# Kernel optimization log

Hardware: AMD Instinct MI355X
Metric: run time of the kernel (lower is better)

Reference implementation:

```python
import jax, jax.numpy as jnp
import numpy as np

B, N, E, C = 1, 100000, 1600000, 128


def setup_inputs() -> dict:
    key = jax.random.key(0)
    k1, k2, k3, k4 = jax.random.split(key, 4)
    x = jax.random.normal(k1, (B, N, C), dtype=jnp.float32)
    edge_index = jax.random.randint(k2, (2, E), 0, N, dtype=jnp.int32)
    W_2 = jax.random.normal(k3, (C,), dtype=jnp.float32)
    W_3 = jax.random.normal(k4, (C,), dtype=jnp.float32)
    return {"x": x, "edge_index": edge_index, "W_2": W_2, "W_3": W_3}


def reference(x, edge_index, W_2, W_3):
    # x: [B, N, C]; edge_index: [2, E] (src, dst)
    src, dst = edge_index[0], edge_index[1]
    num_nodes = x.shape[1]
    # per-edge attention weight: w[b,e] = <(x*W_3)[b,src_e], x[b,dst_e]>
    x3 = (x * W_3)[:, src, :]          # [B, E, C] gather
    x4 = x[:, dst, :]                  # [B, E, C] gather
    w = jnp.einsum('bec,bec->be', x3, x4)  # [B, E]
    # value messages with diagonal W_2 scaling, scattered to destination nodes.
    # Equivalent to out = einsum('bij,bih->bjh', dense_adj(w), x*W_2),
    # where dense_adj[src,dst] = w (to_dense_adj sums duplicate edges; so does segment_sum).
    x2 = x * W_2                       # [B, N, C]
    msg = w[..., None] * x2[:, src, :]  # [B, E, C]
    out = jax.vmap(lambda m: jax.ops.segment_sum(m, dst, num_segments=num_nodes))(msg)
    return out  # [B, N, C]
```

## Files before the change

kernel.cpp:

```cpp
#include <hip/hip_runtime.h>
#include <hip/hip_fp16.h>


#define CCH 128
#define BSHIFT 5
#define BWIDTH 32
#define MAXBIN 4096
#define CH 8192
#define LDSCAP 1280
#define SCAN_BLOCK 256
#define SCAN_ITEMS 4
#define SCAN_TILE (SCAN_BLOCK * SCAN_ITEMS)


__global__ __launch_bounds__(256) void k_pack_hist(
    const float* __restrict__ x, __half* __restrict__ xh, int n4, int nPack,
    const int* __restrict__ dst, int E, int NBIN, int* __restrict__ hist_bm)
{
    __shared__ int cnt[MAXBIN];
    const int tid = threadIdx.x;

    if (blockIdx.x < nPack) {
        const int i = blockIdx.x * 256 + tid;
        if (i < n4) {
            float4 v = reinterpret_cast<const float4*>(x)[i];
            __half2* o = reinterpret_cast<__half2*>(xh) + (size_t)i * 2;
            o[0] = __floats2half2_rn(v.x, v.y);
            o[1] = __floats2half2_rn(v.z, v.w);
        }
        return;
    }

    const int blk = blockIdx.x - nPack;
    for (int b = tid; b < NBIN; b += 256) cnt[b] = 0;
    __syncthreads();

    const int e0 = blk * CH;
    #pragma unroll
    for (int k = 0; k < CH / 1024; ++k) {
        const int g = (e0 >> 2) + k * 256 + tid;
        const int e = g << 2;
        if (e >= E) continue;
        if (e + 4 <= E) {
            const int4 d4 = reinterpret_cast<const int4*>(dst)[g];
            atomicAdd(&cnt[d4.x >> BSHIFT], 1);
            atomicAdd(&cnt[d4.y >> BSHIFT], 1);
            atomicAdd(&cnt[d4.z >> BSHIFT], 1);
            atomicAdd(&cnt[d4.w >> BSHIFT], 1);
        } else {
            for (int ee = e; ee < E; ++ee) atomicAdd(&cnt[dst[ee] >> BSHIFT], 1);
        }
    }
    __syncthreads();
    int* hb = hist_bm + (size_t)blk * NBIN;
    for (int b = tid; b < NBIN; b += 256) hb[b] = cnt[b];
}


__global__ void k_pscan1(const int* __restrict__ hist_bm, int M, int NBIN, int NBLK,
                         int* __restrict__ partial, int* __restrict__ blocksum) {
    __shared__ int sdata[SCAN_BLOCK];
    const int base = blockIdx.x * SCAN_TILE;
    const int t = threadIdx.x;
    int v[SCAN_ITEMS];
    int local = 0;
    #pragma unroll
    for (int k = 0; k < SCAN_ITEMS; ++k) {
        int idx = base + t * SCAN_ITEMS + k;
        int val = 0;
        if (idx < M) {
            int bin = idx / NBLK, blk = idx % NBLK;
            val = hist_bm[(size_t)blk * NBIN + bin];
        }
        v[k] = val;
        local += val;
    }
    sdata[t] = local;
    __syncthreads();
    #pragma unroll
    for (int off = 1; off < SCAN_BLOCK; off <<= 1) {
        int val = (t >= off) ? sdata[t - off] : 0;
        __syncthreads();
        sdata[t] += val;
        __syncthreads();
    }
    const int incl = sdata[t];
    int run = incl - local;
    if (t == SCAN_BLOCK - 1) blocksum[blockIdx.x] = incl;
    #pragma unroll
    for (int k = 0; k < SCAN_ITEMS; ++k) {
        int idx = base + t * SCAN_ITEMS + k;
        if (idx < M) partial[idx] = run;
        run += v[k];
    }
}

__global__ void k_scan2(int* __restrict__ blocksum, int nb) {
    __shared__ int sdata[1024];
    const int t = threadIdx.x;
    const int v = (t < nb) ? blocksum[t] : 0;
    sdata[t] = v;
    __syncthreads();
    for (int off = 1; off < 1024; off <<= 1) {
        int val = (t >= off) ? sdata[t - off] : 0;
        __syncthreads();
        sdata[t] += val;
        __syncthreads();
    }
    if (t < nb) blocksum[t] = sdata[t] - v;
}


__global__ __launch_bounds__(256) void k_place(
    const int* __restrict__ src, const int* __restrict__ dst, int E, int NBIN, int NBLK,
    const int* __restrict__ partial, const int* __restrict__ blocksum,
    unsigned int* __restrict__ coarse)
{
    __shared__ int lcur[MAXBIN];
    const int blk = blockIdx.x;
    const int tid = threadIdx.x;
    for (int b = tid; b < NBIN; b += 256) {
        const size_t idx = (size_t)b * NBLK + blk;
        lcur[b] = partial[idx] + blocksum[idx / SCAN_TILE];
    }
    __syncthreads();

    const int e0 = blk * CH;
    #pragma unroll
    for (int k = 0; k < CH / 1024; ++k) {
        const int g = (e0 >> 2) + k * 256 + tid;
        const int e = g << 2;
        if (e >= E) continue;
        if (e + 4 <= E) {
            const int4 d4 = reinterpret_cast<const int4*>(dst)[g];
            const int4 s4 = reinterpret_cast<const int4*>(src)[g];
            int p;
            p = atomicAdd(&lcur[d4.x >> BSHIFT], 1);
            coarse[p] = (unsigned)s4.x | ((unsigned)(d4.x & (BWIDTH - 1)) << 17);
            p = atomicAdd(&lcur[d4.y >> BSHIFT], 1);
            coarse[p] = (unsigned)s4.y | ((unsigned)(d4.y & (BWIDTH - 1)) << 17);
            p = atomicAdd(&lcur[d4.z >> BSHIFT], 1);
            coarse[p] = (unsigned)s4.z | ((unsigned)(d4.z & (BWIDTH - 1)) << 17);
            p = atomicAdd(&lcur[d4.w >> BSHIFT], 1);
            coarse[p] = (unsigned)s4.w | ((unsigned)(d4.w & (BWIDTH - 1)) << 17);
        } else {
            for (int ee = e; ee < E; ++ee) {
                const int d = dst[ee], s = src[ee];
                int p = atomicAdd(&lcur[d >> BSHIFT], 1);
                coarse[p] = (unsigned)s | ((unsigned)(d & (BWIDTH - 1)) << 17);
            }
        }
    }
}


__global__ __launch_bounds__(256) void k_sort_accum(
    const __half* __restrict__ xh,
    const float* __restrict__ W2,
    const float* __restrict__ W3,
    const unsigned int* __restrict__ coarse,
    const int* __restrict__ partial, const int* __restrict__ blocksum,
    int NBIN, int NBLK, int E, int N,
    float* __restrict__ out)
{
    __shared__ unsigned int raw[LDSCAP];
    __shared__ int srcl[LDSCAP];
    __shared__ int cnt[BWIDTH], offs[BWIDTH], cur[BWIDTH];

    const int bin = blockIdx.x;
    const int tid = threadIdx.x;
    const size_t i0 = (size_t)bin * NBLK;
    const int beg = partial[i0] + blocksum[i0 / SCAN_TILE];
    const int end = (bin + 1 < NBIN)
        ? partial[i0 + NBLK] + blocksum[(i0 + NBLK) / SCAN_TILE] : E;
    const int mtot = end - beg;
    const int m = (mtot < LDSCAP) ? mtot : LDSCAP;

    if (tid < BWIDTH) cnt[tid] = 0;
    __syncthreads();

    for (int i = tid; i < m; i += 256) {
        unsigned u = coarse[beg + i];
        raw[i] = u;
        atomicAdd(&cnt[u >> 17], 1);
    }
    __syncthreads();

    if (tid < BWIDTH) {
        int c = cnt[tid];
        int v = c;
        #pragma unroll
        for (int d2 = 1; d2 < BWIDTH; d2 <<= 1) {
            int t2 = __shfl_up(v, d2, 64);
            if (tid >= d2) v += t2;
        }
        offs[tid] = v - c;
        cur[tid]  = v - c;
    }
    __syncthreads();

    for (int i = tid; i < m; i += 256) {
        unsigned u = raw[i];
        int p = atomicAdd(&cur[u >> 17], 1);
        srcl[p] = (int)(u & 0x1FFFFu);
    }
    __syncthreads();

    const int lane = tid & 63;
    const int grp  = lane >> 4;
    const int sl   = lane & 15;
    const int gid  = (tid >> 6) * 4 + grp;

    const float4 w3a = *reinterpret_cast<const float4*>(W3 + sl * 8);
    const float4 w3b = *reinterpret_cast<const float4*>(W3 + sl * 8 + 4);
    const float4 w2a = *reinterpret_cast<const float4*>(W2 + sl * 8);
    const float4 w2b = *reinterpret_cast<const float4*>(W2 + sl * 8 + 4);

    const char* xb = (const char*)xh;
    const int choff = sl << 4;

    #pragma unroll
    for (int i = 0; i < BWIDTH / 16; ++i) {
        const int dl = gid * (BWIDTH / 16) + i;
        const int node = (bin << BSHIFT) + dl;
        if (node < N) {
            union { int4 i4; __half2 h[4]; } uD;
            uD.i4 = *reinterpret_cast<const int4*>(xb + (((size_t)node) << 8) + choff);
            const float2 e0 = __half22float2(uD.h[0]);
            const float2 e1 = __half22float2(uD.h[1]);
            const float2 e2 = __half22float2(uD.h[2]);
            const float2 e3 = __half22float2(uD.h[3]);
            const float4 va = make_float4(w3a.x * e0.x, w3a.y * e0.y,
                                          w3a.z * e1.x, w3a.w * e1.y);
            const float4 vb = make_float4(w3b.x * e2.x, w3b.y * e2.y,
                                          w3b.z * e3.x, w3b.w * e3.y);

            float4 accA = make_float4(0.f, 0.f, 0.f, 0.f);
            float4 accB = make_float4(0.f, 0.f, 0.f, 0.f);

            const int b0 = offs[dl];
            const int c  = cnt[dl];

            int j = 0;
            for (; j + 4 <= c; j += 4) {
                const int s0 = srcl[b0 + j];
                const int s1 = srcl[b0 + j + 1];
                const int s2 = srcl[b0 + j + 2];
                const int s3 = srcl[b0 + j + 3];
                union { int4 i4; __half2 h[4]; } u0, u1, u2, u3;
                u0.i4 = *reinterpret_cast<const int4*>(xb + (((size_t)s0) << 8) + choff);
                u1.i4 = *reinterpret_cast<const int4*>(xb + (((size_t)s1) << 8) + choff);
                u2.i4 = *reinterpret_cast<const int4*>(xb + (((size_t)s2) << 8) + choff);
                u3.i4 = *reinterpret_cast<const int4*>(xb + (((size_t)s3) << 8) + choff);
                const float2 f00 = __half22float2(u0.h[0]);
                const float2 f01 = __half22float2(u0.h[1]);
                const float2 f02 = __half22float2(u0.h[2]);
                const float2 f03 = __half22float2(u0.h[3]);
                const float2 f10 = __half22float2(u1.h[0]);
                const float2 f11 = __half22float2(u1.h[1]);
                const float2 f12 = __half22float2(u1.h[2]);
                const float2 f13 = __half22float2(u1.h[3]);
                const float2 f20 = __half22float2(u2.h[0]);
                const float2 f21 = __half22float2(u2.h[1]);
                const float2 f22 = __half22float2(u2.h[2]);
                const float2 f23 = __half22float2(u2.h[3]);
                const float2 f30 = __half22float2(u3.h[0]);
                const float2 f31 = __half22float2(u3.h[1]);
                const float2 f32 = __half22float2(u3.h[2]);
                const float2 f33 = __half22float2(u3.h[3]);
                float p0 = f00.x * va.x + f00.y * va.y + f01.x * va.z + f01.y * va.w
                         + f02.x * vb.x + f02.y * vb.y + f03.x * vb.z + f03.y * vb.w;
                float p1 = f10.x * va.x + f10.y * va.y + f11.x * va.z + f11.y * va.w
                         + f12.x * vb.x + f12.y * vb.y + f13.x * vb.z + f13.y * vb.w;
                float p2 = f20.x * va.x + f20.y * va.y + f21.x * va.z + f21.y * va.w
                         + f22.x * vb.x + f22.y * vb.y + f23.x * vb.z + f23.y * vb.w;
                float p3 = f30.x * va.x + f30.y * va.y + f31.x * va.z + f31.y * va.w
                         + f32.x * vb.x + f32.y * vb.y + f33.x * vb.z + f33.y * vb.w;
                #pragma unroll
                for (int off = 1; off < 16; off <<= 1) {
                    p0 += __shfl_xor(p0, off, 64);
                    p1 += __shfl_xor(p1, off, 64);
                    p2 += __shfl_xor(p2, off, 64);
                    p3 += __shfl_xor(p3, off, 64);
                }
                accA.x += p0 * f00.x + p1 * f10.x + p2 * f20.x + p3 * f30.x;
                accA.y += p0 * f00.y + p1 * f10.y + p2 * f20.y + p3 * f30.y;
                accA.z += p0 * f01.x + p1 * f11.x + p2 * f21.x + p3 * f31.x;
                accA.w += p0 * f01.y + p1 * f11.y + p2 * f21.y + p3 * f31.y;
                accB.x += p0 * f02.x + p1 * f12.x + p2 * f22.x + p3 * f32.x;
                accB.y += p0 * f02.y + p1 * f12.y + p2 * f22.y + p3 * f32.y;
                accB.z += p0 * f03.x + p1 * f13.x + p2 * f23.x + p3 * f33.x;
                accB.w += p0 * f03.y + p1 * f13.y + p2 * f23.y + p3 * f33.y;
            }
            for (; j < c; ++j) {
                const int s0 = srcl[b0 + j];
                union { int4 i4; __half2 h[4]; } u0;
                u0.i4 = *reinterpret_cast<const int4*>(xb + (((size_t)s0) << 8) + choff);
                const float2 f0 = __half22float2(u0.h[0]);
                const float2 f1 = __half22float2(u0.h[1]);
                const float2 f2 = __half22float2(u0.h[2]);
                const float2 f3 = __half22float2(u0.h[3]);
                float p = f0.x * va.x + f0.y * va.y + f1.x * va.z + f1.y * va.w
                        + f2.x * vb.x + f2.y * vb.y + f3.x * vb.z + f3.y * vb.w;
                #pragma unroll
                for (int off = 1; off < 16; off <<= 1) p += __shfl_xor(p, off, 64);
                accA.x += p * f0.x;
                accA.y += p * f0.y;
                accA.z += p * f1.x;
                accA.w += p * f1.y;
                accB.x += p * f2.x;
                accB.y += p * f2.y;
                accB.z += p * f3.x;
                accB.w += p * f3.y;
            }
            for (int i2 = LDSCAP; i2 < mtot; ++i2) {
                const unsigned u = coarse[beg + i2];
                if ((int)(u >> 17) != dl) continue;
                const int s0 = (int)(u & 0x1FFFFu);
                union { int4 i4; __half2 h[4]; } u0;
                u0.i4 = *reinterpret_cast<const int4*>(xb + (((size_t)s0) << 8) + choff);
                const float2 f0 = __half22float2(u0.h[0]);
                const float2 f1 = __half22float2(u0.h[1]);
                const float2 f2 = __half22float2(u0.h[2]);
                const float2 f3 = __half22float2(u0.h[3]);
                float p = f0.x * va.x + f0.y * va.y + f1.x * va.z + f1.y * va.w
                        + f2.x * vb.x + f2.y * vb.y + f3.x * vb.z + f3.y * vb.w;
                #pragma unroll
                for (int off = 1; off < 16; off <<= 1) p += __shfl_xor(p, off, 64);
                accA.x += p * f0.x;
                accA.y += p * f0.y;
                accA.z += p * f1.x;
                accA.w += p * f1.y;
                accB.x += p * f2.x;
                accB.y += p * f2.y;
                accB.z += p * f3.x;
                accB.w += p * f3.y;
            }

            accA.x *= w2a.x; accA.y *= w2a.y; accA.z *= w2a.z; accA.w *= w2a.w;
            accB.x *= w2b.x; accB.y *= w2b.y; accB.z *= w2b.z; accB.w *= w2b.w;
            float* orow = out + (size_t)node * CCH + sl * 8;
            *reinterpret_cast<float4*>(orow)     = accA;
            *reinterpret_cast<float4*>(orow + 4) = accB;
        }
    }
}


__global__ __launch_bounds__(256) void edge_gather_scatter(
    const float* __restrict__ x, const int* __restrict__ edge_index,
    const float* __restrict__ W2, const float* __restrict__ W3,
    float* __restrict__ out, int E)
{
    const int e    = (blockIdx.x * blockDim.x + threadIdx.x) >> 6;
    const int lane = threadIdx.x & 63;
    if (e >= E) return;
    const int s = edge_index[e];
    const int d = edge_index[E + e];
    const float2 xs = *reinterpret_cast<const float2*>(x + (size_t)s * CCH + lane * 2);
    const float2 xd = *reinterpret_cast<const float2*>(x + (size_t)d * CCH + lane * 2);
    const float2 w3 = *reinterpret_cast<const float2*>(W3 + lane * 2);
    const float2 w2 = *reinterpret_cast<const float2*>(W2 + lane * 2);
    float p = xs.x * w3.x * xd.x + xs.y * w3.y * xd.y;
    #pragma unroll
    for (int off = 32; off > 0; off >>= 1) p += __shfl_xor(p, off, 64);
    float* o = out + (size_t)d * CCH + lane * 2;
    atomicAdd(o,     p * xs.x * w2.x);
    atomicAdd(o + 1, p * xs.y * w2.y);
}


extern "C" void kernel_launch(void* const* d_in, const int* in_sizes, int n_in,
                              void* d_out, int out_size, void* d_ws, size_t ws_size,
                              hipStream_t stream) {
    const float* x          = (const float*)d_in[0];
    const int*   edge_index = (const int*)  d_in[1];
    const float* W2         = (const float*)d_in[2];
    const float* W3         = (const float*)d_in[3];
    float*       out        = (float*)d_out;

    const int E = in_sizes[1] / 2;
    const int N = out_size / CCH;
    const int* src = edge_index;
    const int* dst = edge_index + E;

    const int NBIN = (N + BWIDTH - 1) >> BSHIFT;
    const int NBLK = (E + CH - 1) / CH;
    const long long Mll = (long long)NBIN * NBLK;
    const int M = (int)Mll;
    const int nb1 = (M + SCAN_TILE - 1) / SCAN_TILE;

    const size_t xh_bytes = (size_t)N * CCH * 2;
    const size_t need = xh_bytes + (size_t)E * 4 + 2 * (size_t)M * 4 + 1024 * 4;

    const bool aligned16 = (((uintptr_t)src & 15) == 0) && (((uintptr_t)dst & 15) == 0);

    if (N <= (1 << 17) && NBIN <= MAXBIN && Mll <= (1LL << 20) && nb1 <= 1024 &&
        aligned16 && ws_size >= need) {
        char* base = (char*)d_ws;
        __half* xh       = (__half*)base;        base += xh_bytes;
        unsigned* coarse = (unsigned*)base;      base += (size_t)E * 4;
        int* hist_bm     = (int*)base;           base += (size_t)M * 4;
        int* partial     = (int*)base;           base += (size_t)M * 4;
        int* blocksum    = (int*)base;

        const int n4 = N * CCH / 4;
        const int nPack = (n4 + 255) / 256;

        k_pack_hist<<<nPack + NBLK, 256, 0, stream>>>(x, xh, n4, nPack,
                                                      dst, E, NBIN, hist_bm);
        k_pscan1<<<nb1, SCAN_BLOCK, 0, stream>>>(hist_bm, M, NBIN, NBLK, partial, blocksum);
        k_scan2<<<1, 1024, 0, stream>>>(blocksum, nb1);
        k_place<<<NBLK, 256, 0, stream>>>(src, dst, E, NBIN, NBLK,
                                          partial, blocksum, coarse);
        k_sort_accum<<<NBIN, 256, 0, stream>>>(xh, W2, W3, coarse,
                                               partial, blocksum,
                                               NBIN, NBLK, E, N, out);
        return;
    }

    hipMemsetAsync(d_out, 0, (size_t)out_size * sizeof(float), stream);
    const int grid = (E * 64 + 255) / 256;
    edge_gather_scatter<<<grid, 256, 0, stream>>>(x, edge_index, W2, W3, out, E);
}
```

Measured before the change: 125.5 us.

## Tile bin-major histogram scan through LDS and deepen gather batching in accumulate

The first-level scan now loads a 16-bin by NBLK tile of the block-major histogram into shared memory, so global reads stay coalesced and each block's offsets match whole bins, replacing the strided index/divide access. The sort-accumulate kernel uses per-wave counters for its LDS counting sort to cut atomic contention. It also prefetches the destination rows before the sort phase and batches eight source-row gathers per iteration for more memory parallelism, with a two-blocks-per-CU launch bound. A new NBLK cap adds a guard on the fast path, and the wider batch raises register pressure.

```diff
diff --git a/kernel.cpp b/kernel.cpp
--- a/kernel.cpp
+++ b/kernel.cpp
@@ -8,9 +8,8 @@
 #define MAXBIN 4096
 #define CH 8192
 #define LDSCAP 1280
-#define SCAN_BLOCK 256
-#define SCAN_ITEMS 4
-#define SCAN_TILE (SCAN_BLOCK * SCAN_ITEMS)
+#define TBINS 16
+#define NBLKCAP 256
 
 
 __global__ __launch_bounds__(256) void k_pack_hist(
@@ -57,28 +56,38 @@
 }
 
 
-__global__ void k_pscan1(const int* __restrict__ hist_bm, int M, int NBIN, int NBLK,
-                         int* __restrict__ partial, int* __restrict__ blocksum) {
-    __shared__ int sdata[SCAN_BLOCK];
-    const int base = blockIdx.x * SCAN_TILE;
+__global__ __launch_bounds__(256) void k_pscan1(
+    const int* __restrict__ hist_bm, int NBIN, int NBLK,
+    int* __restrict__ partial, int* __restrict__ blocksum)
+{
+    __shared__ int tile[TBINS][NBLKCAP + 1];
+    __shared__ int sdata[256];
     const int t = threadIdx.x;
-    int v[SCAN_ITEMS];
+    const int B0 = blockIdx.x * TBINS;
+
+    for (int g = t; g < TBINS * (NBLKCAP + 1); g += 256)
+        (&tile[0][0])[g] = 0;
+    __syncthreads();
+
+    for (int g = t; g < NBLK * TBINS; g += 256) {
+        const int blk = g >> 4;
+        const int tb  = g & (TBINS - 1);
+        const int bin = B0 + tb;
+        if (bin < NBIN) tile[tb][blk] = hist_bm[(size_t)blk * NBIN + bin];
+    }
+    __syncthreads();
+
+    const int tb  = t >> 4;
+    const int bk0 = (t & 15) * 16;
+    int v[16];
     int local = 0;
     #pragma unroll
-    for (int k = 0; k < SCAN_ITEMS; ++k) {
-        int idx = base + t * SCAN_ITEMS + k;
-        int val = 0;
-        if (idx < M) {
-            int bin = idx / NBLK, blk = idx % NBLK;
-            val = hist_bm[(size_t)blk * NBIN + bin];
-        }
-        v[k] = val;
-        local += val;
-    }
+    for (int k = 0; k < 16; ++k) { v[k] = tile[tb][bk0 + k]; local += v[k]; }
+
     sdata[t] = local;
     __syncthreads();
     #pragma unroll
-    for (int off = 1; off < SCAN_BLOCK; off <<= 1) {
+    for (int off = 1; off < 256; off <<= 1) {
         int val = (t >= off) ? sdata[t - off] : 0;
         __syncthreads();
         sdata[t] += val;
@@ -86,12 +95,16 @@
     }
     const int incl = sdata[t];
     int run = incl - local;
-    if (t == SCAN_BLOCK - 1) blocksum[blockIdx.x] = incl;
-    #pragma unroll
-    for (int k = 0; k < SCAN_ITEMS; ++k) {
-        int idx = base + t * SCAN_ITEMS + k;
-        if (idx < M) partial[idx] = run;
-        run += v[k];
+    if (t == 255) blocksum[blockIdx.x] = incl;
+
+    const int bin = B0 + tb;
+    if (bin < NBIN) {
+        #pragma unroll
+        for (int k = 0; k < 16; ++k) {
+            const int blk = bk0 + k;
+            if (blk < NBLK) partial[(size_t)bin * NBLK + blk] = run;
+            run += v[k];
+        }
     }
 }
 
@@ -120,8 +133,7 @@
     const int blk = blockIdx.x;
     const int tid = threadIdx.x;
     for (int b = tid; b < NBIN; b += 256) {
-        const size_t idx = (size_t)b * NBLK + blk;
-        lcur[b] = partial[idx] + blocksum[idx / SCAN_TILE];
+        lcur[b] = partial[(size_t)b * NBLK + blk] + blocksum[b / TBINS];
     }
     __syncthreads();
 
@@ -154,7 +166,7 @@
 }
 
 
-__global__ __launch_bounds__(256) void k_sort_accum(
+__global__ __launch_bounds__(256, 2) void k_sort_accum(
     const __half* __restrict__ xh,
     const float* __restrict__ W2,
     const float* __restrict__ W3,
@@ -165,184 +177,204 @@
 {
     __shared__ unsigned int raw[LDSCAP];
     __shared__ int srcl[LDSCAP];
-    __shared__ int cnt[BWIDTH], offs[BWIDTH], cur[BWIDTH];
-
-    const int bin = blockIdx.x;
-    const int tid = threadIdx.x;
+    __shared__ int cnt4[4][BWIDTH];
+    __shared__ int cur4[4][BWIDTH];
+    __shared__ int offs[BWIDTH], cnt[BWIDTH];
+
+    const int bin  = blockIdx.x;
+    const int tid  = threadIdx.x;
+    const int wv   = tid >> 6;
+    const int lane = tid & 63;
+    const int grp  = lane >> 4;
+    const int sl   = lane & 15;
+    const int gid  = wv * 4 + grp;
+    const int choff = sl << 4;
+    const char* xb = (const char*)xh;
+
+    union H { int4 i4; __half2 h[4]; };
+
+    const int node0 = (bin << BSHIFT) + gid * 2;
+    const int node1 = node0 + 1;
+    H uD0, uD1;
+    uD0.i4 = make_int4(0, 0, 0, 0);
+    uD1.i4 = make_int4(0, 0, 0, 0);
+    if (node0 < N) uD0.i4 = *reinterpret_cast<const int4*>(xb + (((size_t)node0) << 8) + choff);
+    if (node1 < N) uD1.i4 = *reinterpret_cast<const int4*>(xb + (((size_t)node1) << 8) + choff);
+
     const size_t i0 = (size_t)bin * NBLK;
-    const int beg = partial[i0] + blocksum[i0 / SCAN_TILE];
+    const int beg = partial[i0] + blocksum[bin / TBINS];
     const int end = (bin + 1 < NBIN)
-        ? partial[i0 + NBLK] + blocksum[(i0 + NBLK) / SCAN_TILE] : E;
+        ? partial[i0 + NBLK] + blocksum[(bin + 1) / TBINS] : E;
     const int mtot = end - beg;
     const int m = (mtot < LDSCAP) ? mtot : LDSCAP;
 
-    if (tid < BWIDTH) cnt[tid] = 0;
+    if (tid < 4 * BWIDTH) (&cnt4[0][0])[tid] = 0;
     __syncthreads();
 
     for (int i = tid; i < m; i += 256) {
         unsigned u = coarse[beg + i];
         raw[i] = u;
-        atomicAdd(&cnt[u >> 17], 1);
+        atomicAdd(&cnt4[wv][u >> 17], 1);
     }
     __syncthreads();
 
     if (tid < BWIDTH) {
-        int c = cnt[tid];
-        int v = c;
+        const int c0 = cnt4[0][tid], c1 = cnt4[1][tid];
+        const int c2 = cnt4[2][tid], c3 = cnt4[3][tid];
+        const int tot = c0 + c1 + c2 + c3;
+        int v = tot;
         #pragma unroll
         for (int d2 = 1; d2 < BWIDTH; d2 <<= 1) {
             int t2 = __shfl_up(v, d2, 64);
             if (tid >= d2) v += t2;
         }
-        offs[tid] = v - c;
-        cur[tid]  = v - c;
+        const int ex = v - tot;
+        offs[tid] = ex;
+        cnt[tid]  = tot;
+        cur4[0][tid] = ex;
+        cur4[1][tid] = ex + c0;
+        cur4[2][tid] = ex + c0 + c1;
+        cur4[3][tid] = ex + c0 + c1 + c2;
     }
     __syncthreads();
 
     for (int i = tid; i < m; i += 256) {
-        unsigned u = raw[i];
-        int p = atomicAdd(&cur[u >> 17], 1);
+        const unsigned u = raw[i];
+        const int p = atomicAdd(&cur4[wv][u >> 17], 1);
         srcl[p] = (int)(u & 0x1FFFFu);
     }
     __syncthreads();
-
-    const int lane = tid & 63;
-    const int grp  = lane >> 4;
-    const int sl   = lane & 15;
-    const int gid  = (tid >> 6) * 4 + grp;
 
     const float4 w3a = *reinterpret_cast<const float4*>(W3 + sl * 8);
     const float4 w3b = *reinterpret_cast<const float4*>(W3 + sl * 8 + 4);
     const float4 w2a = *reinterpret_cast<const float4*>(W2 + sl * 8);
     const float4 w2b = *reinterpret_cast<const float4*>(W2 + sl * 8 + 4);
 
-    const char* xb = (const char*)xh;
-    const int choff = sl << 4;
-
-    #pragma unroll
-    for (int i = 0; i < BWIDTH / 16; ++i) {
-        const int dl = gid * (BWIDTH / 16) + i;
-        const int node = (bin << BSHIFT) + dl;
-        if (node < N) {
-            union { int4 i4; __half2 h[4]; } uD;
-            uD.i4 = *reinterpret_cast<const int4*>(xb + (((size_t)node) << 8) + choff);
-            const float2 e0 = __half22float2(uD.h[0]);
-            const float2 e1 = __half22float2(uD.h[1]);
-            const float2 e2 = __half22float2(uD.h[2]);
-            const float2 e3 = __half22float2(uD.h[3]);
-            const float4 va = make_float4(w3a.x * e0.x, w3a.y * e0.y,
-                                          w3a.z * e1.x, w3a.w * e1.y);
-            const float4 vb = make_float4(w3b.x * e2.x, w3b.y * e2.y,
-                                          w3b.z * e3.x, w3b.w * e3.y);
-
-            float4 accA = make_float4(0.f, 0.f, 0.f, 0.f);
-            float4 accB = make_float4(0.f, 0.f, 0.f, 0.f);
-
-            const int b0 = offs[dl];
-            const int c  = cnt[dl];
-
-            int j = 0;
-            for (; j + 4 <= c; j += 4) {
-                const int s0 = srcl[b0 + j];
-                const int s1 = srcl[b0 + j + 1];
-                const int s2 = srcl[b0 + j + 2];
-                const int s3 = srcl[b0 + j + 3];
-                union { int4 i4; __half2 h[4]; } u0, u1, u2, u3;
-                u0.i4 = *reinterpret_cast<const int4*>(xb + (((size_t)s0) << 8) + choff);
-                u1.i4 = *reinterpret_cast<const int4*>(xb + (((size_t)s1) << 8) + choff);
-                u2.i4 = *reinterpret_cast<const int4*>(xb + (((size_t)s2) << 8) + choff);
-                u3.i4 = *reinterpret_cast<const int4*>(xb + (((size_t)s3) << 8) + choff);
-                const float2 f00 = __half22float2(u0.h[0]);
-                const float2 f01 = __half22float2(u0.h[1]);
-                const float2 f02 = __half22float2(u0.h[2]);
-                const float2 f03 = __half22float2(u0.h[3]);
-                const float2 f10 = __half22float2(u1.h[0]);
-                const float2 f11 = __half22float2(u1.h[1]);
-                const float2 f12 = __half22float2(u1.h[2]);
-                const float2 f13 = __half22float2(u1.h[3]);
-                const float2 f20 = __half22float2(u2.h[0]);
-                const float2 f21 = __half22float2(u2.h[1]);
-                const float2 f22 = __half22float2(u2.h[2]);
-                const float2 f23 = __half22float2(u2.h[3]);
-                const float2 f30 = __half22float2(u3.h[0]);
-                const float2 f31 = __half22float2(u3.h[1]);
-                const float2 f32 = __half22float2(u3.h[2]);
-                const float2 f33 = __half22float2(u3.h[3]);
-                float p0 = f00.x * va.x + f00.y * va.y + f01.x * va.z + f01.y * va.w
-                         + f02.x * vb.x + f02.y * vb.y + f03.x * vb.z + f03.y * vb.w;
-                float p1 = f10.x * va.x + f10.y * va.y + f11.x * va.z + f11.y * va.w
-                         + f12.x * vb.x + f12.y * vb.y + f13.x * vb.z + f13.y * vb.w;
-                float p2 = f20.x * va.x + f20.y * va.y + f21.x * va.z + f21.y * va.w
-                         + f22.x * vb.x + f22.y * vb.y + f23.x * vb.z + f23.y * vb.w;
-                float p3 = f30.x * va.x + f30.y * va.y + f31.x * va.z + f31.y * va.w
-                         + f32.x * vb.x + f32.y * vb.y + f33.x * vb.z + f33.y * vb.w;
+    #pragma unroll
+    for (int i = 0; i < 2; ++i) {
+        const int node = (i == 0) ? node0 : node1;
+        if (node >= N) continue;
+        const int dl = gid * 2 + i;
+        const H uD = (i == 0) ? uD0 : uD1;
+
+        const float2 e0 = __half22float2(uD.h[0]);
+        const float2 e1 = __half22float2(uD.h[1]);
+        const float2 e2 = __half22float2(uD.h[2]);
+        const float2 e3 = __half22float2(uD.h[3]);
+        const float4 va = make_float4(w3a.x * e0.x, w3a.y * e0.y,
+                                      w3a.z * e1.x, w3a.w * e1.y);
+        const float4 vb = make_float4(w3b.x * e2.x, w3b.y * e2.y,
+                                      w3b.z * e3.x, w3b.w * e3.y);
+
+        float4 accA = make_float4(0.f, 0.f, 0.f, 0.f);
+        float4 accB = make_float4(0.f, 0.f, 0.f, 0.f);
+
+        const int b0 = offs[dl];
+        const int c  = cnt[dl];
+
+        int j = 0;
+        for (; j + 8 <= c; j += 8) {
+            H q[8];
+            #pragma unroll
+            for (int k = 0; k < 8; ++k)
+                q[k].i4 = *reinterpret_cast<const int4*>(
+                    xb + (((size_t)srcl[b0 + j + k]) << 8) + choff);
+            float2 f0[8], f1[8], f2[8], f3[8];
+            float p[8];
+            #pragma unroll
+            for (int k = 0; k < 8; ++k) {
+                f0[k] = __half22float2(q[k].h[0]);
+                f1[k] = __half22float2(q[k].h[1]);
+                f2[k] = __half22float2(q[k].h[2]);
+                f3[k] = __half22float2(q[k].h[3]);
+                p[k] = f0[k].x * va.x + f0[k].y * va.y + f1[k].x * va.z + f1[k].y * va.w
+                     + f2[k].x * vb.x + f2[k].y * vb.y + f3[k].x * vb.z + f3[k].y * vb.w;
+            }
+            #pragma unroll
+            for (int off = 1; off < 16; off <<= 1) {
                 #pragma unroll
-                for (int off = 1; off < 16; off <<= 1) {
-                    p0 += __shfl_xor(p0, off, 64);
-                    p1 += __shfl_xor(p1, off, 64);
-                    p2 += __shfl_xor(p2, off, 64);
-                    p3 += __shfl_xor(p3, off, 64);
-                }
-                accA.x += p0 * f00.x + p1 * f10.x + p2 * f20.x + p3 * f30.x;
-                accA.y += p0 * f00.y + p1 * f10.y + p2 * f20.y + p3 * f30.y;
-                accA.z += p0 * f01.x + p1 * f11.x + p2 * f21.x + p3 * f31.x;
-                accA.w += p0 * f01.y + p1 * f11.y + p2 * f21.y + p3 * f31.y;
-                accB.x += p0 * f02.x + p1 * f12.x + p2 * f22.x + p3 * f32.x;
-                accB.y += p0 * f02.y + p1 * f12.y + p2 * f22.y + p3 * f32.y;
-                accB.z += p0 * f03.x + p1 * f13.x + p2 * f23.x + p3 * f33.x;
-                accB.w += p0 * f03.y + p1 * f13.y + p2 * f23.y + p3 * f33.y;
-            }
-            for (; j < c; ++j) {
-                const int s0 = srcl[b0 + j];
-                union { int4 i4; __half2 h[4]; } u0;
-                u0.i4 = *reinterpret_cast<const int4*>(xb + (((size_t)s0) << 8) + choff);
-                const float2 f0 = __half22float2(u0.h[0]);
-                const float2 f1 = __half22float2(u0.h[1]);
-                const float2 f2 = __half22float2(u0.h[2]);
-                const float2 f3 = __half22float2(u0.h[3]);
-                float p = f0.x * va.x + f0.y * va.y + f1.x * va.z + f1.y * va.w
-                        + f2.x * vb.x + f2.y * vb.y + f3.x * vb.z + f3.y * vb.w;
+                for (int k = 0; k < 8; ++k) p[k] += __shfl_xor(p[k], off, 64);
+            }
+            #pragma unroll
+            for (int k = 0; k < 8; ++k) {
+                accA.x += p[k] * f0[k].x; accA.y += p[k] * f0[k].y;
+                accA.z += p[k] * f1[k].x; accA.w += p[k] * f1[k].y;
+                accB.x += p[k] * f2[k].x; accB.y += p[k] * f2[k].y;
+                accB.z += p[k] * f3[k].x; accB.w += p[k] * f3[k].y;
+            }
+        }
+        for (; j + 4 <= c; j += 4) {
+            H q[4];
+            #pragma unroll
+            for (int k = 0; k < 4; ++k)
+                q[k].i4 = *reinterpret_cast<const int4*>(
+                    xb + (((size_t)srcl[b0 + j + k]) << 8) + choff);
+            float2 f0[4], f1[4], f2[4], f3[4];
+            float p[4];
+            #pragma unroll
+            for (int k = 0; k < 4; ++k) {
+                f0[k] = __half22float2(q[k].h[0]);
+                f1[k] = __half22float2(q[k].h[1]);
+                f2[k] = __half22float2(q[k].h[2]);
+                f3[k] = __half22float2(q[k].h[3]);
+                p[k] = f0[k].x * va.x + f0[k].y * va.y + f1[k].x * va.z + f1[k].y * va.w
+                     + f2[k].x * vb.x + f2[k].y * vb.y + f3[k].x * vb.z + f3[k].y * vb.w;
+            }
+            #pragma unroll
+            for (int off = 1; off < 16; off <<= 1) {
                 #pragma unroll
-                for (int off = 1; off < 16; off <<= 1) p += __shfl_xor(p, off, 64);
-                accA.x += p * f0.x;
-                accA.y += p * f0.y;
-                accA.z += p * f1.x;
-                accA.w += p * f1.y;
-                accB.x += p * f2.x;
-                accB.y += p * f2.y;
-                accB.z += p * f3.x;
-                accB.w += p * f3.y;
-            }
-            for (int i2 = LDSCAP; i2 < mtot; ++i2) {
-                const unsigned u = coarse[beg + i2];
-                if ((int)(u >> 17) != dl) continue;
-                const int s0 = (int)(u & 0x1FFFFu);
-                union { int4 i4; __half2 h[4]; } u0;
-                u0.i4 = *reinterpret_cast<const int4*>(xb + (((size_t)s0) << 8) + choff);
-                const float2 f0 = __half22float2(u0.h[0]);
-                const float2 f1 = __half22float2(u0.h[1]);
-                const float2 f2 = __half22float2(u0.h[2]);
-                const float2 f3 = __half22float2(u0.h[3]);
-                float p = f0.x * va.x + f0.y * va.y + f1.x * va.z + f1.y * va.w
-                        + f2.x * vb.x + f2.y * vb.y + f3.x * vb.z + f3.y * vb.w;
-                #pragma unroll
-                for (int off = 1; off < 16; off <<= 1) p += __shfl_xor(p, off, 64);
-                accA.x += p * f0.x;
-                accA.y += p * f0.y;
-                accA.z += p * f1.x;
-                accA.w += p * f1.y;
-                accB.x += p * f2.x;
-                accB.y += p * f2.y;
-                accB.z += p * f3.x;
-                accB.w += p * f3.y;
-            }
-
-            accA.x *= w2a.x; accA.y *= w2a.y; accA.z *= w2a.z; accA.w *= w2a.w;
-            accB.x *= w2b.x; accB.y *= w2b.y; accB.z *= w2b.z; accB.w *= w2b.w;
-            float* orow = out + (size_t)node * CCH + sl * 8;
-            *reinterpret_cast<float4*>(orow)     = accA;
-            *reinterpret_cast<float4*>(orow + 4) = accB;
-        }
+                for (int k = 0; k < 4; ++k) p[k] += __shfl_xor(p[k], off, 64);
+            }
+            #pragma unroll
+            for (int k = 0; k < 4; ++k) {
+                accA.x += p[k] * f0[k].x; accA.y += p[k] * f0[k].y;
+                accA.z += p[k] * f1[k].x; accA.w += p[k] * f1[k].y;
+                accB.x += p[k] * f2[k].x; accB.y += p[k] * f2[k].y;
+                accB.z += p[k] * f3[k].x; accB.w += p[k] * f3[k].y;
+            }
+        }
+        for (; j < c; ++j) {
+            H u0;
+            u0.i4 = *reinterpret_cast<const int4*>(
+                xb + (((size_t)srcl[b0 + j]) << 8) + choff);
+            const float2 f0 = __half22float2(u0.h[0]);
+            const float2 f1 = __half22float2(u0.h[1]);
+            const float2 f2 = __half22float2(u0.h[2]);
+            const float2 f3 = __half22float2(u0.h[3]);
+            float p = f0.x * va.x + f0.y * va.y + f1.x * va.z + f1.y * va.w
+                    + f2.x * vb.x + f2.y * vb.y + f3.x * vb.z + f3.y * vb.w;
+            #pragma unroll
+            for (int off = 1; off < 16; off <<= 1) p += __shfl_xor(p, off, 64);
+            accA.x += p * f0.x; accA.y += p * f0.y;
+            accA.z += p * f1.x; accA.w += p * f1.y;
+            accB.x += p * f2.x; accB.y += p * f2.y;
+            accB.z += p * f3.x; accB.w += p * f3.y;
+        }
+        for (int i2 = LDSCAP; i2 < mtot; ++i2) {
+            const unsigned u = coarse[beg + i2];
+            if ((int)(u >> 17) != dl) continue;
+            H u0;
+            u0.i4 = *reinterpret_cast<const int4*>(
+                xb + (((size_t)(u & 0x1FFFFu)) << 8) + choff);
+            const float2 f0 = __half22float2(u0.h[0]);
+            const float2 f1 = __half22float2(u0.h[1]);
+            const float2 f2 = __half22float2(u0.h[2]);
+            const float2 f3 = __half22float2(u0.h[3]);
+            float p = f0.x * va.x + f0.y * va.y + f1.x * va.z + f1.y * va.w
+                    + f2.x * vb.x + f2.y * vb.y + f3.x * vb.z + f3.y * vb.w;
+            #pragma unroll
+            for (int off = 1; off < 16; off <<= 1) p += __shfl_xor(p, off, 64);
+            accA.x += p * f0.x; accA.y += p * f0.y;
+            accA.z += p * f1.x; accA.w += p * f1.y;
+            accB.x += p * f2.x; accB.y += p * f2.y;
+            accB.z += p * f3.x; accB.w += p * f3.y;
+        }
+
+        accA.x *= w2a.x; accA.y *= w2a.y; accA.z *= w2a.z; accA.w *= w2a.w;
+        accB.x *= w2b.x; accB.y *= w2b.y; accB.z *= w2b.z; accB.w *= w2b.w;
+        float* orow = out + (size_t)node * CCH + sl * 8;
+        *reinterpret_cast<float4*>(orow)     = accA;
+        *reinterpret_cast<float4*>(orow + 4) = accB;
     }
 }
 
@@ -388,15 +420,15 @@
     const int NBLK = (E + CH - 1) / CH;
     const long long Mll = (long long)NBIN * NBLK;
     const int M = (int)Mll;
-    const int nb1 = (M + SCAN_TILE - 1) / SCAN_TILE;
+    const int nb1 = (NBIN + TBINS - 1) / TBINS;
 
     const size_t xh_bytes = (size_t)N * CCH * 2;
     const size_t need = xh_bytes + (size_t)E * 4 + 2 * (size_t)M * 4 + 1024 * 4;
 
     const bool aligned16 = (((uintptr_t)src & 15) == 0) && (((uintptr_t)dst & 15) == 0);
 
-    if (N <= (1 << 17) && NBIN <= MAXBIN && Mll <= (1LL << 20) && nb1 <= 1024 &&
-        aligned16 && ws_size >= need) {
+    if (N <= (1 << 17) && NBIN <= MAXBIN && NBLK <= NBLKCAP && Mll <= (1LL << 20) &&
+        nb1 <= 1024 && aligned16 && ws_size >= need) {
         char* base = (char*)d_ws;
         __half* xh       = (__half*)base;        base += xh_bytes;
         unsigned* coarse = (unsigned*)base;      base += (size_t)E * 4;
@@ -409,7 +441,7 @@
 
         k_pack_hist<<<nPack + NBLK, 256, 0, stream>>>(x, xh, n4, nPack,
                                                       dst, E, NBIN, hist_bm);
-        k_pscan1<<<nb1, SCAN_BLOCK, 0, stream>>>(hist_bm, M, NBIN, NBLK, partial, blocksum);
+        k_pscan1<<<nb1, 256, 0, stream>>>(hist_bm, NBIN, NBLK, partial, blocksum);
         k_scan2<<<1, 1024, 0, stream>>>(blocksum, nb1);
         k_place<<<NBLK, 256, 0, stream>>>(src, dst, E, NBIN, NBLK,
                                           partial, blocksum, coarse);
```

Result: slower. 130.4 us (+3.9%).

## Replace two-pass scan with single-pass decoupled look-back scan and prefetch dst rows

Applied to the files above, without the earlier changes.

The two-kernel prefix scan (per-tile scan plus a single-block scan of block sums) becomes one kernel. It stages a 16-bin by NBLK tile of the histogram in LDS for coalesced reads and chains tiles with a decoupled look-back over a status array, which is zeroed by an added memset. Consumers now read one scanned array instead of adding partial and blocksum. The accumulate kernel issues its two destination-row loads before the LDS bucket sort so their latency overlaps it. The look-back relies on forward progress across earlier blocks, and a new NBLK cap narrows when the fast path is taken.

```diff
diff --git a/kernel.cpp b/kernel.cpp
--- a/kernel.cpp
+++ b/kernel.cpp
@@ -8,9 +8,8 @@
 #define MAXBIN 4096
 #define CH 8192
 #define LDSCAP 1280
-#define SCAN_BLOCK 256
-#define SCAN_ITEMS 4
-#define SCAN_TILE (SCAN_BLOCK * SCAN_ITEMS)
+#define TBINS 16
+#define NBLKCAP 256
 
 
 __global__ __launch_bounds__(256) void k_pack_hist(
@@ -57,72 +56,89 @@
 }
 
 
-__global__ void k_pscan1(const int* __restrict__ hist_bm, int M, int NBIN, int NBLK,
-                         int* __restrict__ partial, int* __restrict__ blocksum) {
-    __shared__ int sdata[SCAN_BLOCK];
-    const int base = blockIdx.x * SCAN_TILE;
+__global__ __launch_bounds__(256) void k_pscan(
+    const int* __restrict__ hist_bm, int NBIN, int NBLK, int E_unused,
+    int* __restrict__ scanned, unsigned int* __restrict__ status)
+{
+    __shared__ int tile[TBINS][NBLKCAP + 1];
+    __shared__ int sdata[256];
+    __shared__ int sbase;
     const int t = threadIdx.x;
-    int v[SCAN_ITEMS];
+    const int B0 = blockIdx.x * TBINS;
+
+    for (int g = t; g < TBINS * (NBLKCAP + 1); g += 256)
+        (&tile[0][0])[g] = 0;
+    __syncthreads();
+
+    for (int g = t; g < NBLK * TBINS; g += 256) {
+        const int blk = g >> 4;
+        const int tb  = g & (TBINS - 1);
+        const int bin = B0 + tb;
+        if (bin < NBIN) tile[tb][blk] = hist_bm[(size_t)blk * NBIN + bin];
+    }
+    __syncthreads();
+
+    const int tb  = t >> 4;
+    const int bk0 = (t & 15) * 16;
+    int v[16];
     int local = 0;
     #pragma unroll
-    for (int k = 0; k < SCAN_ITEMS; ++k) {
-        int idx = base + t * SCAN_ITEMS + k;
-        int val = 0;
-        if (idx < M) {
-            int bin = idx / NBLK, blk = idx % NBLK;
-            val = hist_bm[(size_t)blk * NBIN + bin];
-        }
-        v[k] = val;
-        local += val;
-    }
+    for (int k = 0; k < 16; ++k) { v[k] = tile[tb][bk0 + k]; local += v[k]; }
+
     sdata[t] = local;
     __syncthreads();
     #pragma unroll
-    for (int off = 1; off < SCAN_BLOCK; off <<= 1) {
+    for (int off = 1; off < 256; off <<= 1) {
         int val = (t >= off) ? sdata[t - off] : 0;
         __syncthreads();
         sdata[t] += val;
         __syncthreads();
     }
     const int incl = sdata[t];
-    int run = incl - local;
-    if (t == SCAN_BLOCK - 1) blocksum[blockIdx.x] = incl;
-    #pragma unroll
-    for (int k = 0; k < SCAN_ITEMS; ++k) {
-        int idx = base + t * SCAN_ITEMS + k;
-        if (idx < M) partial[idx] = run;
-        run += v[k];
-    }
-}
-
-__global__ void k_scan2(int* __restrict__ blocksum, int nb) {
-    __shared__ int sdata[1024];
-    const int t = threadIdx.x;
-    const int v = (t < nb) ? blocksum[t] : 0;
-    sdata[t] = v;
-    __syncthreads();
-    for (int off = 1; off < 1024; off <<= 1) {
-        int val = (t >= off) ? sdata[t - off] : 0;
-        __syncthreads();
-        sdata[t] += val;
-        __syncthreads();
-    }
-    if (t < nb) blocksum[t] = sdata[t] - v;
+    const int total = sdata[255];
+
+    if (t == 0) {
+        __hip_atomic_store(&status[blockIdx.x], (1u << 30) | (unsigned)total,
+                           __ATOMIC_RELAXED, __HIP_MEMORY_SCOPE_AGENT);
+        int base = 0;
+        for (int j = (int)blockIdx.x - 1; j >= 0; --j) {
+            unsigned w;
+            do {
+                w = __hip_atomic_load(&status[j], __ATOMIC_RELAXED,
+                                      __HIP_MEMORY_SCOPE_AGENT);
+            } while ((w >> 30) == 0u);
+            base += (int)(w & 0x3FFFFFFFu);
+            if ((w >> 30) == 2u) break;
+        }
+        __hip_atomic_store(&status[blockIdx.x],
+                           (2u << 30) | (unsigned)(base + total),
+                           __ATOMIC_RELAXED, __HIP_MEMORY_SCOPE_AGENT);
+        sbase = base;
+    }
+    __syncthreads();
+
+    int run = sbase + (incl - local);
+    const int bin = B0 + tb;
+    if (bin < NBIN) {
+        #pragma unroll
+        for (int k = 0; k < 16; ++k) {
+            const int blk = bk0 + k;
+            if (blk < NBLK) scanned[(size_t)bin * NBLK + blk] = run;
+            run += v[k];
+        }
+    }
 }
 
 
 __global__ __launch_bounds__(256) void k_place(
     const int* __restrict__ src, const int* __restrict__ dst, int E, int NBIN, int NBLK,
-    const int* __restrict__ partial, const int* __restrict__ blocksum,
-    unsigned int* __restrict__ coarse)
+    const int* __restrict__ scanned, unsigned int* __restrict__ coarse)
 {
     __shared__ int lcur[MAXBIN];
     const int blk = blockIdx.x;
     const int tid = threadIdx.x;
-    for (int b = tid; b < NBIN; b += 256) {
-        const size_t idx = (size_t)b * NBLK + blk;
-        lcur[b] = partial[idx] + blocksum[idx / SCAN_TILE];
-    }
+    for (int b = tid; b < NBIN; b += 256)
+        lcur[b] = scanned[(size_t)b * NBLK + blk];
     __syncthreads();
 
     const int e0 = blk * CH;
@@ -159,7 +175,7 @@
     const float* __restrict__ W2,
     const float* __restrict__ W3,
     const unsigned int* __restrict__ coarse,
-    const int* __restrict__ partial, const int* __restrict__ blocksum,
+    const int* __restrict__ scanned,
     int NBIN, int NBLK, int E, int N,
     float* __restrict__ out)
 {
@@ -167,12 +183,28 @@
     __shared__ int srcl[LDSCAP];
     __shared__ int cnt[BWIDTH], offs[BWIDTH], cur[BWIDTH];
 
-    const int bin = blockIdx.x;
-    const int tid = threadIdx.x;
+    const int bin  = blockIdx.x;
+    const int tid  = threadIdx.x;
+    const int lane = tid & 63;
+    const int grp  = lane >> 4;
+    const int sl   = lane & 15;
+    const int gid  = (tid >> 6) * 4 + grp;
+    const int choff = sl << 4;
+    const char* xb = (const char*)xh;
+
+    union H { int4 i4; __half2 h[4]; };
+
+    const int node0 = (bin << BSHIFT) + gid * 2;
+    const int node1 = node0 + 1;
+    H uD0, uD1;
+    uD0.i4 = make_int4(0, 0, 0, 0);
+    uD1.i4 = make_int4(0, 0, 0, 0);
+    if (node0 < N) uD0.i4 = *reinterpret_cast<const int4*>(xb + (((size_t)node0) << 8) + choff);
+    if (node1 < N) uD1.i4 = *reinterpret_cast<const int4*>(xb + (((size_t)node1) << 8) + choff);
+
     const size_t i0 = (size_t)bin * NBLK;
-    const int beg = partial[i0] + blocksum[i0 / SCAN_TILE];
-    const int end = (bin + 1 < NBIN)
-        ? partial[i0 + NBLK] + blocksum[(i0 + NBLK) / SCAN_TILE] : E;
+    const int beg = scanned[i0];
+    const int end = (bin + 1 < NBIN) ? scanned[i0 + NBLK] : E;
     const int mtot = end - beg;
     const int m = (mtot < LDSCAP) ? mtot : LDSCAP;
 
@@ -200,149 +232,132 @@
     __syncthreads();
 
     for (int i = tid; i < m; i += 256) {
-        unsigned u = raw[i];
-        int p = atomicAdd(&cur[u >> 17], 1);
+        const unsigned u = raw[i];
+        const int p = atomicAdd(&cur[u >> 17], 1);
         srcl[p] = (int)(u & 0x1FFFFu);
     }
     __syncthreads();
-
-    const int lane = tid & 63;
-    const int grp  = lane >> 4;
-    const int sl   = lane & 15;
-    const int gid  = (tid >> 6) * 4 + grp;
 
     const float4 w3a = *reinterpret_cast<const float4*>(W3 + sl * 8);
     const float4 w3b = *reinterpret_cast<const float4*>(W3 + sl * 8 + 4);
     const float4 w2a = *reinterpret_cast<const float4*>(W2 + sl * 8);
     const float4 w2b = *reinterpret_cast<const float4*>(W2 + sl * 8 + 4);
 
-    const char* xb = (const char*)xh;
-    const int choff = sl << 4;
-
-    #pragma unroll
-    for (int i = 0; i < BWIDTH / 16; ++i) {
-        const int dl = gid * (BWIDTH / 16) + i;
-        const int node = (bin << BSHIFT) + dl;
-        if (node < N) {
-            union { int4 i4; __half2 h[4]; } uD;
-            uD.i4 = *reinterpret_cast<const int4*>(xb + (((size_t)node) << 8) + choff);
-            const float2 e0 = __half22float2(uD.h[0]);
-            const float2 e1 = __half22float2(uD.h[1]);
-            const float2 e2 = __half22float2(uD.h[2]);
-            const float2 e3 = __half22float2(uD.h[3]);
-            const float4 va = make_float4(w3a.x * e0.x, w3a.y * e0.y,
-                                          w3a.z * e1.x, w3a.w * e1.y);
-            const float4 vb = make_float4(w3b.x * e2.x, w3b.y * e2.y,
-                                          w3b.z * e3.x, w3b.w * e3.y);
-
-            float4 accA = make_float4(0.f, 0.f, 0.f, 0.f);
-            float4 accB = make_float4(0.f, 0.f, 0.f, 0.f);
-
-            const int b0 = offs[dl];
-            const int c  = cnt[dl];
-
-            int j = 0;
-            for (; j + 4 <= c; j += 4) {
-                const int s0 = srcl[b0 + j];
-                const int s1 = srcl[b0 + j + 1];
-                const int s2 = srcl[b0 + j + 2];
-                const int s3 = srcl[b0 + j + 3];
-                union { int4 i4; __half2 h[4]; } u0, u1, u2, u3;
-                u0.i4 = *reinterpret_cast<const int4*>(xb + (((size_t)s0) << 8) + choff);
-                u1.i4 = *reinterpret_cast<const int4*>(xb + (((size_t)s1) << 8) + choff);
-                u2.i4 = *reinterpret_cast<const int4*>(xb + (((size_t)s2) << 8) + choff);
-                u3.i4 = *reinterpret_cast<const int4*>(xb + (((size_t)s3) << 8) + choff);
-                const float2 f00 = __half22float2(u0.h[0]);
-                const float2 f01 = __half22float2(u0.h[1]);
-                const float2 f02 = __half22float2(u0.h[2]);
-                const float2 f03 = __half22float2(u0.h[3]);
-                const float2 f10 = __half22float2(u1.h[0]);
-                const float2 f11 = __half22float2(u1.h[1]);
-                const float2 f12 = __half22float2(u1.h[2]);
-                const float2 f13 = __half22float2(u1.h[3]);
-                const float2 f20 = __half22float2(u2.h[0]);
-                const float2 f21 = __half22float2(u2.h[1]);
-                const float2 f22 = __half22float2(u2.h[2]);
-                const float2 f23 = __half22float2(u2.h[3]);
-                const float2 f30 = __half22float2(u3.h[0]);
-                const float2 f31 = __half22float2(u3.h[1]);
-                const float2 f32 = __half22float2(u3.h[2]);
-                const float2 f33 = __half22float2(u3.h[3]);
-                float p0 = f00.x * va.x + f00.y * va.y + f01.x * va.z + f01.y * va.w
-                         + f02.x * vb.x + f02.y * vb.y + f03.x * vb.z + f03.y * vb.w;
-                float p1 = f10.x * va.x + f10.y * va.y + f11.x * va.z + f11.y * va.w
-                         + f12.x * vb.x + f12.y * vb.y + f13.x * vb.z + f13.y * vb.w;
-                float p2 = f20.x * va.x + f20.y * va.y + f21.x * va.z + f21.y * va.w
-                         + f22.x * vb.x + f22.y * vb.y + f23.x * vb.z + f23.y * vb.w;
-                float p3 = f30.x * va.x + f30.y * va.y + f31.x * va.z + f31.y * va.w
-                         + f32.x * vb.x + f32.y * vb.y + f33.x * vb.z + f33.y * vb.w;
-                #pragma unroll
-                for (int off = 1; off < 16; off <<= 1) {
-                    p0 += __shfl_xor(p0, off, 64);
-                    p1 += __shfl_xor(p1, off, 64);
-                    p2 += __shfl_xor(p2, off, 64);
-                    p3 += __shfl_xor(p3, off, 64);
-                }
-                accA.x += p0 * f00.x + p1 * f10.x + p2 * f20.x + p3 * f30.x;
-                accA.y += p0 * f00.y + p1 * f10.y + p2 * f20.y + p3 * f30.y;
-                accA.z += p0 * f01.x + p1 * f11.x + p2 * f21.x + p3 * f31.x;
-                accA.w += p0 * f01.y + p1 * f11.y + p2 * f21.y + p3 * f31.y;
-                accB.x += p0 * f02.x + p1 * f12.x + p2 * f22.x + p3 * f32.x;
-                accB.y += p0 * f02.y + p1 * f12.y + p2 * f22.y + p3 * f32.y;
-                accB.z += p0 * f03.x + p1 * f13.x + p2 * f23.x + p3 * f33.x;
-                accB.w += p0 * f03.y + p1 * f13.y + p2 * f23.y + p3 * f33.y;
+    #pragma unroll
+    for (int i = 0; i < 2; ++i) {
+        const int node = (i == 0) ? node0 : node1;
+        if (node >= N) continue;
+        const int dl = gid * 2 + i;
+        const H uD = (i == 0) ? uD0 : uD1;
+
+        const float2 e0 = __half22float2(uD.h[0]);
+        const float2 e1 = __half22float2(uD.h[1]);
+        const float2 e2 = __half22float2(uD.h[2]);
+        const float2 e3 = __half22float2(uD.h[3]);
+        const float4 va = make_float4(w3a.x * e0.x, w3a.y * e0.y,
+                                      w3a.z * e1.x, w3a.w * e1.y);
+        const float4 vb = make_float4(w3b.x * e2.x, w3b.y * e2.y,
+                                      w3b.z * e3.x, w3b.w * e3.y);
+
+        float4 accA = make_float4(0.f, 0.f, 0.f, 0.f);
+        float4 accB = make_float4(0.f, 0.f, 0.f, 0.f);
+
+        const int b0 = offs[dl];
+        const int c  = cnt[dl];
+
+        int j = 0;
+        for (; j + 4 <= c; j += 4) {
+            const int s0 = srcl[b0 + j];
+            const int s1 = srcl[b0 + j + 1];
+            const int s2 = srcl[b0 + j + 2];
+            const int s3 = srcl[b0 + j + 3];
+            H u0, u1, u2, u3;
+            u0.i4 = *reinterpret_cast<const int4*>(xb + (((size_t)s0) << 8) + choff);
+            u1.i4 = *reinterpret_cast<const int4*>(xb + (((size_t)s1) << 8) + choff);
+            u2.i4 = *reinterpret_cast<const int4*>(xb + (((size_t)s2) << 8) + choff);
+            u3.i4 = *reinterpret_cast<const int4*>(xb + (((size_t)s3) << 8) + choff);
+            const float2 f00 = __half22float2(u0.h[0]);
+            const float2 f01 = __half22float2(u0.h[1]);
+            const float2 f02 = __half22float2(u0.h[2]);
+            const float2 f03 = __half22float2(u0.h[3]);
+            const float2 f10 = __half22float2(u1.h[0]);
+            const float2 f11 = __half22float2(u1.h[1]);
+            const float2 f12 = __half22float2(u1.h[2]);
+            const float2 f13 = __half22float2(u1.h[3]);
+            const float2 f20 = __half22float2(u2.h[0]);
+            const float2 f21 = __half22float2(u2.h[1]);
+            const float2 f22 = __half22float2(u2.h[2]);
+            const float2 f23 = __half22float2(u2.h[3]);
+            const float2 f30 = __half22float2(u3.h[0]);
+            const float2 f31 = __half22float2(u3.h[1]);
+            const float2 f32 = __half22float2(u3.h[2]);
+            const float2 f33 = __half22float2(u3.h[3]);
+            float p0 = f00.x * va.x + f00.y * va.y + f01.x * va.z + f01.y * va.w
+                     + f02.x * vb.x + f02.y * vb.y + f03.x * vb.z + f03.y * vb.w;
+            float p1 = f10.x * va.x + f10.y * va.y + f11.x * va.z + f11.y * va.w
+                     + f12.x * vb.x + f12.y * vb.y + f13.x * vb.z + f13.y * vb.w;
+            float p2 = f20.x * va.x + f20.y * va.y + f21.x * va.z + f21.y * va.w
+                     + f22.x * vb.x + f22.y * vb.y + f23.x * vb.z + f23.y * vb.w;
+            float p3 = f30.x * va.x + f30.y * va.y + f31.x * va.z + f31.y * va.w
+                     + f32.x * vb.x + f32.y * vb.y + f33.x * vb.z + f33.y * vb.w;
+            #pragma unroll
+            for (int off = 1; off < 16; off <<= 1) {
+                p0 += __shfl_xor(p0, off, 64);
+                p1 += __shfl_xor(p1, off, 64);
+                p2 += __shfl_xor(p2, off, 64);
+                p3 += __shfl_xor(p3, off, 64);
             }
-            for (; j < c; ++j) {
-                const int s0 = srcl[b0 + j];
-                union { int4 i4; __half2 h[4]; } u0;
-                u0.i4 = *reinterpret_cast<const int4*>(xb + (((size_t)s0) << 8) + choff);
-                const float2 f0 = __half22float2(u0.h[0]);
-                const float2 f1 = __half22float2(u0.h[1]);
-                const float2 f2 = __half22float2(u0.h[2]);
-                const float2 f3 = __half22float2(u0.h[3]);
-                float p = f0.x * va.x + f0.y * va.y + f1.x * va.z + f1.y * va.w
-                        + f2.x * vb.x + f2.y * vb.y + f3.x * vb.z + f3.y * vb.w;
-                #pragma unroll
-                for (int off = 1; off < 16; off <<= 1) p += __shfl_xor(p, off, 64);
-                accA.x += p * f0.x;
-                accA.y += p * f0.y;
-                accA.z += p * f1.x;
-                accA.w += p * f1.y;
-                accB.x += p * f2.x;
-                accB.y += p * f2.y;
-                accB.z += p * f3.x;
-                accB.w += p * f3.y;
-            }
-            for (int i2 = LDSCAP; i2 < mtot; ++i2) {
-                const unsigned u = coarse[beg + i2];
-                if ((int)(u >> 17) != dl) continue;
-                const int s0 = (int)(u & 0x1FFFFu);
-                union { int4 i4; __half2 h[4]; } u0;
-                u0.i4 = *reinterpret_cast<const int4*>(xb + (((size_t)s0) << 8) + choff);
-                const float2 f0 = __half22float2(u0.h[0]);
-                const float2 f1 = __half22float2(u0.h[1]);
-                const float2 f2 = __half22float2(u0.h[2]);
-                const float2 f3 = __half22float2(u0.h[3]);
-                float p = f0.x * va.x + f0.y * va.y + f1.x * va.z + f1.y * va.w
-                        + f2.x * vb.x + f2.y * vb.y + f3.x * vb.z + f3.y * vb.w;
-                #pragma unroll
-                for (int off = 1; off < 16; off <<= 1) p += __shfl_xor(p, off, 64);
-                accA.x += p * f0.x;
-                accA.y += p * f0.y;
-                accA.z += p * f1.x;
-                accA.w += p * f1.y;
-                accB.x += p * f2.x;
-                accB.y += p * f2.y;
-                accB.z += p * f3.x;
-                accB.w += p * f3.y;
-            }
-
-            accA.x *= w2a.x; accA.y *= w2a.y; accA.z *= w2a.z; accA.w *= w2a.w;
-            accB.x *= w2b.x; accB.y *= w2b.y; accB.z *= w2b.z; accB.w *= w2b.w;
-            float* orow = out + (size_t)node * CCH + sl * 8;
-            *reinterpret_cast<float4*>(orow)     = accA;
-            *reinterpret_cast<float4*>(orow + 4) = accB;
-        }
+            accA.x += p0 * f00.x + p1 * f10.x + p2 * f20.x + p3 * f30.x;
+            accA.y += p0 * f00.y + p1 * f10.y + p2 * f20.y + p3 * f30.y;
+            accA.z += p0 * f01.x + p1 * f11.x + p2 * f21.x + p3 * f31.x;
+            accA.w += p0 * f01.y + p1 * f11.y + p2 * f21.y + p3 * f31.y;
+            accB.x += p0 * f02.x + p1 * f12.x + p2 * f22.x + p3 * f32.x;
+            accB.y += p0 * f02.y + p1 * f12.y + p2 * f22.y + p3 * f32.y;
+            accB.z += p0 * f03.x + p1 * f13.x + p2 * f23.x + p3 * f33.x;
+            accB.w += p0 * f03.y + p1 * f13.y + p2 * f23.y + p3 * f33.y;
+        }
+        for (; j < c; ++j) {
+            H u0;
+            u0.i4 = *reinterpret_cast<const int4*>(
+                xb + (((size_t)srcl[b0 + j]) << 8) + choff);
+            const float2 f0 = __half22float2(u0.h[0]);
+            const float2 f1 = __half22float2(u0.h[1]);
+            const float2 f2 = __half22float2(u0.h[2]);
+            const float2 f3 = __half22float2(u0.h[3]);
+            float p = f0.x * va.x + f0.y * va.y + f1.x * va.z + f1.y * va.w
+                    + f2.x * vb.x + f2.y * vb.y + f3.x * vb.z + f3.y * vb.w;
+            #pragma unroll
+            for (int off = 1; off < 16; off <<= 1) p += __shfl_xor(p, off, 64);
+            accA.x += p * f0.x; accA.y += p * f0.y;
+            accA.z += p * f1.x; accA.w += p * f1.y;
+            accB.x += p * f2.x; accB.y += p * f2.y;
+            accB.z += p * f3.x; accB.w += p * f3.y;
+        }
+        for (int i2 = LDSCAP; i2 < mtot; ++i2) {
+            const unsigned u = coarse[beg + i2];
+            if ((int)(u >> 17) != dl) continue;
+            H u0;
+            u0.i4 = *reinterpret_cast<const int4*>(
+                xb + (((size_t)(u & 0x1FFFFu)) << 8) + choff);
+            const float2 f0 = __half22float2(u0.h[0]);
+            const float2 f1 = __half22float2(u0.h[1]);
+            const float2 f2 = __half22float2(u0.h[2]);
+            const float2 f3 = __half22float2(u0.h[3]);
+            float p = f0.x * va.x + f0.y * va.y + f1.x * va.z + f1.y * va.w
+                    + f2.x * vb.x + f2.y * vb.y + f3.x * vb.z + f3.y * vb.w;
+            #pragma unroll
+            for (int off = 1; off < 16; off <<= 1) p += __shfl_xor(p, off, 64);
+            accA.x += p * f0.x; accA.y += p * f0.y;
+            accA.z += p * f1.x; accA.w += p * f1.y;
+            accB.x += p * f2.x; accB.y += p * f2.y;
+            accB.z += p * f3.x; accB.w += p * f3.y;
+        }
+
+        accA.x *= w2a.x; accA.y *= w2a.y; accA.z *= w2a.z; accA.w *= w2a.w;
+        accB.x *= w2b.x; accB.y *= w2b.y; accB.z *= w2b.z; accB.w *= w2b.w;
+        float* orow = out + (size_t)node * CCH + sl * 8;
+        *reinterpret_cast<float4*>(orow)     = accA;
+        *reinterpret_cast<float4*>(orow + 4) = accB;
     }
 }
 
@@ -388,33 +403,31 @@
     const int NBLK = (E + CH - 1) / CH;
     const long long Mll = (long long)NBIN * NBLK;
     const int M = (int)Mll;
-    const int nb1 = (M + SCAN_TILE - 1) / SCAN_TILE;
+    const int nb1 = (NBIN + TBINS - 1) / TBINS;
 
     const size_t xh_bytes = (size_t)N * CCH * 2;
-    const size_t need = xh_bytes + (size_t)E * 4 + 2 * (size_t)M * 4 + 1024 * 4;
+    const size_t need = xh_bytes + (size_t)E * 4 + 2 * (size_t)M * 4 + 4096;
 
     const bool aligned16 = (((uintptr_t)src & 15) == 0) && (((uintptr_t)dst & 15) == 0);
 
-    if (N <= (1 << 17) && NBIN <= MAXBIN && Mll <= (1LL << 20) && nb1 <= 1024 &&
-        aligned16 && ws_size >= need) {
+    if (N <= (1 << 17) && NBIN <= MAXBIN && NBLK <= NBLKCAP && Mll <= (1LL << 20) &&
+        nb1 <= 1024 && aligned16 && ws_size >= need) {
         char* base = (char*)d_ws;
-        __half* xh       = (__half*)base;        base += xh_bytes;
-        unsigned* coarse = (unsigned*)base;      base += (size_t)E * 4;
-        int* hist_bm     = (int*)base;           base += (size_t)M * 4;
-        int* partial     = (int*)base;           base += (size_t)M * 4;
-        int* blocksum    = (int*)base;
+        __half* xh        = (__half*)base;       base += xh_bytes;
+        unsigned* coarse  = (unsigned*)base;     base += (size_t)E * 4;
+        int* hist_bm      = (int*)base;          base += (size_t)M * 4;
+        int* scanned      = (int*)base;          base += (size_t)M * 4;
+        unsigned* status  = (unsigned*)base;
 
         const int n4 = N * CCH / 4;
         const int nPack = (n4 + 255) / 256;
 
+        hipMemsetAsync(status, 0, 1024 * sizeof(unsigned), stream);
         k_pack_hist<<<nPack + NBLK, 256, 0, stream>>>(x, xh, n4, nPack,
                                                       dst, E, NBIN, hist_bm);
-        k_pscan1<<<nb1, SCAN_BLOCK, 0, stream>>>(hist_bm, M, NBIN, NBLK, partial, blocksum);
-        k_scan2<<<1, 1024, 0, stream>>>(blocksum, nb1);
-        k_place<<<NBLK, 256, 0, stream>>>(src, dst, E, NBIN, NBLK,
-                                          partial, blocksum, coarse);
-        k_sort_accum<<<NBIN, 256, 0, stream>>>(xh, W2, W3, coarse,
-                                               partial, blocksum,
+        k_pscan<<<nb1, 256, 0, stream>>>(hist_bm, NBIN, NBLK, E, scanned, status);
+        k_place<<<NBLK, 256, 0, stream>>>(src, dst, E, NBIN, NBLK, scanned, coarse);
+        k_sort_accum<<<NBIN, 256, 0, stream>>>(xh, W2, W3, coarse, scanned,
                                                NBIN, NBLK, E, N, out);
         return;
     }
```

After: 139.3 us. 1.11x slower.
